# Performance work log

Measured on AMD Instinct MI355X. Metric: run time of the kernel, lower is better.

The kernel has to match this reference:

```python
import jax, jax.numpy as jnp
import numpy as np

B = 64
D_MODEL = 2048
D_SSM = 4096      # expand * d_model
HEADDIM = 64
NHEADS = 64       # D_SSM // HEADDIM
D_STATE = 128
D_IN_PROJ = 2 * D_SSM + 2 * D_STATE + NHEADS  # 8512, d_mlp == 0
ACT_LEVELS = 2 ** (8 - 1) - 1  # 127
W_LEVELS = 2 ** (8 - 1) - 1


def fake_quant(x, levels):
    # symmetric absmax fake-quant along last dim with straight-through estimator
    scale = jnp.max(jnp.abs(x), axis=-1, keepdims=True) / levels
    scale = jnp.where(scale == 0, 1.0, scale)
    q = jnp.round(x / scale) * scale
    return x + jax.lax.stop_gradient(q - x)


def quant_linear(x, W):
    # QuantLinear: fake-quant activations (per row) and weights (per output channel)
    xq = fake_quant(x, ACT_LEVELS)
    Wq = fake_quant(W, W_LEVELS)
    return xq @ Wq.T


def softplus_taylor3(x):
    return jnp.log(2.0) + 0.5 * x + x ** 2 / 8.0 + x ** 3 / 48.0


def exp_taylor5(x):
    return 1.0 + x + x ** 2 / 2.0 + x ** 3 / 6.0 + x ** 4 / 24.0 + x ** 5 / 120.0


def setup_inputs() -> dict:
    key = jax.random.key(0)
    k = jax.random.split(key, 7)
    hidden_states = jax.random.normal(k[0], (B, 1, D_MODEL), dtype=jnp.float32)
    ssm_state = jax.random.normal(k[1], (B, NHEADS, HEADDIM, D_STATE), dtype=jnp.float32) * 0.1
    W_in = jax.random.normal(k[2], (D_IN_PROJ, D_MODEL), dtype=jnp.float32) * (1.0 / np.sqrt(D_MODEL))
    # dt_bias = inverse-softplus of dt ~ LogUniform(1e-3, 1e-1)
    dt = jnp.exp(jax.random.uniform(k[3], (NHEADS,)) * (np.log(0.1) - np.log(0.001)) + np.log(0.001))
    dt_bias = dt + jnp.log(-jnp.expm1(-dt))
    A_log = jnp.log(jax.random.uniform(k[4], (NHEADS,), minval=1.0, maxval=16.0))
    Dp = jnp.ones((D_SSM,), dtype=jnp.float32)
    W_out = jax.random.normal(k[5], (D_MODEL, D_SSM), dtype=jnp.float32) * (1.0 / np.sqrt(D_SSM))
    return {"hidden_states": hidden_states, "ssm_state": ssm_state, "W_in": W_in,
            "dt_bias": dt_bias, "A_log": A_log, "D": Dp, "W_out": W_out}


def reference(hidden_states, ssm_state, W_in, dt_bias, A_log, D, W_out):
    dtype = hidden_states.dtype
    b = hidden_states.shape[0]
    zxbcdt = quant_linear(hidden_states[:, 0, :], W_in)  # [b, 8512]
    z = zxbcdt[:, :D_SSM]
    xBC = zxbcdt[:, D_SSM:2 * D_SSM + 2 * D_STATE]
    dt = zxbcdt[:, -NHEADS:]
    # activation fake-quant on xBC (STE)
    xBC = fake_quant(xBC, ACT_LEVELS)
    x = xBC[:, :D_SSM]                                   # [b, d_ssm]
    Bm = xBC[:, D_SSM:D_SSM + D_STATE]                   # [b, n]
    C = xBC[:, D_SSM + D_STATE:]                         # [b, n]
    A = -jnp.exp(A_log.astype(jnp.float32))              # [h]
    # no_sftplus: piecewise 3rd-order Taylor softplus
    dt = dt + dt_bias.astype(dt.dtype)
    dt = jnp.where(dt < -2.0, 0.0, jnp.where(dt > 2.0, dt, softplus_taylor3(dt)))
    # taylor_exp: clipped 5th-order Taylor exp of dt*A
    dA = jnp.maximum(dt * A, -10000.0)
    scale = jnp.clip(exp_taylor5(dA), 0.0, 1.0)          # [b, h]
    xh = x.reshape(b, NHEADS, HEADDIM)                   # [b, h, p]
    dBx = jnp.einsum('bh,bn,bhp->bhpn', dt, Bm, xh)
    ssm_state = ssm_state * scale[:, :, None, None] + dBx  # [b, h, p, n]
    y = jnp.einsum('bhpn,bn->bhp', ssm_state.astype(dtype), C).reshape(b, D_SSM)
    y = fake_quant(y, ACT_LEVELS)
    y = y + D.astype(dtype) * x                          # per-channel skip (D has d_ssm entries)
    y = y * jax.nn.relu(z)
    y = fake_quant(y, ACT_LEVELS)
    out = quant_linear(y, W_out)                         # [b, d_model]
    return out[:, None, :]
```

## Files before the change

### kernel.cpp

```cpp
#include <hip/hip_runtime.h>


#define B_       64
#define DMODEL   2048
#define DSSM     4096
#define NH       64
#define HD       64
#define DSTATE   128
#define DPROJ    8512
#define XBCLEN   4352

typedef __attribute__((ext_vector_type(8))) short short8;
typedef __attribute__((ext_vector_type(4))) float floatx4;

__device__ __forceinline__ float blockMax256(float v, float* sm) {
  #pragma unroll
  for (int off = 32; off > 0; off >>= 1)
    v = fmaxf(v, __shfl_xor(v, off, 64));
  __syncthreads();
  if ((threadIdx.x & 63) == 0) sm[threadIdx.x >> 6] = v;
  __syncthreads();
  return fmaxf(fmaxf(sm[0], sm[1]), fmaxf(sm[2], sm[3]));
}

__device__ __forceinline__ unsigned short bf16_of_int(float q) {
  return (unsigned short)(__float_as_uint(q) >> 16);
}

template<int COLS>
__global__ __launch_bounds__(256) void quant_rows(const float* __restrict__ in,
                                                  unsigned short* __restrict__ outq,
                                                  float* __restrict__ scales) {
  __shared__ float sm[4];
  constexpr int NV = COLS / 1024;
  int r = blockIdx.x;
  const float4* row = (const float4*)(in + (size_t)r * COLS);
  float4 v[NV];
  float m = 0.f;
  #pragma unroll
  for (int i = 0; i < NV; i++) {
    v[i] = row[threadIdx.x + i * 256];
    m = fmaxf(m, fmaxf(fmaxf(fabsf(v[i].x), fabsf(v[i].y)),
                       fmaxf(fabsf(v[i].z), fabsf(v[i].w))));
  }
  float s = blockMax256(m, sm) * (1.0f / 127.0f);
  if (s == 0.f) s = 1.f;
  if (threadIdx.x == 0) scales[r] = s;
  unsigned short* orow = outq + (size_t)r * COLS;
  #pragma unroll
  for (int i = 0; i < NV; i++) {
    int idx = (threadIdx.x + i * 256) * 4;
    ushort4 o;
    o.x = bf16_of_int(rintf(v[i].x / s));
    o.y = bf16_of_int(rintf(v[i].y / s));
    o.z = bf16_of_int(rintf(v[i].z / s));
    o.w = bf16_of_int(rintf(v[i].w / s));
    *(ushort4*)(orow + idx) = o;
  }
}

__global__ __launch_bounds__(256) void gemm_q(
    const unsigned short* __restrict__ A, int lda, const float* __restrict__ sA,
    const unsigned short* __restrict__ Bq, int ldb, const float* __restrict__ sB,
    float* __restrict__ Cout, int N, int kchunk) {
  int wave = threadIdx.x >> 6;
  int lane = threadIdx.x & 63;
  int l16 = lane & 15, quad = lane >> 4;
  int n0 = blockIdx.x * 64 + wave * 16;
  int k0 = blockIdx.y * kchunk;
  floatx4 zero = {0.f, 0.f, 0.f, 0.f};
  floatx4 acc[4] = {zero, zero, zero, zero};
  const unsigned short* brow = Bq + (size_t)(n0 + l16) * ldb;
  for (int k = k0; k < k0 + kchunk; k += 32) {
    int koff = k + quad * 8;
    short8 bfrag = *(const short8*)(brow + koff);
    #pragma unroll
    for (int mt = 0; mt < 4; mt++) {
      short8 afrag = *(const short8*)(A + (size_t)(mt * 16 + l16) * lda + koff);
      acc[mt] = __builtin_amdgcn_mfma_f32_16x16x32_bf16(afrag, bfrag, acc[mt], 0, 0, 0);
    }
  }
  int ncol = n0 + l16;
  float sb = sB[ncol];
  #pragma unroll
  for (int mt = 0; mt < 4; mt++) {
    #pragma unroll
    for (int r = 0; r < 4; r++) {
      int m = mt * 16 + quad * 4 + r;
      atomicAdd(&Cout[(size_t)m * N + ncol], acc[mt][r] * sA[m] * sb);
    }
  }
}

__global__ __launch_bounds__(256) void kxbc(const float* __restrict__ zxb,
                                            float* __restrict__ xbcq) {
  __shared__ float sm[4];
  int b = blockIdx.x;
  const float* row = zxb + (size_t)b * DPROJ + DSSM;
  float4 v[5];
  float m = 0.f;
  #pragma unroll
  for (int i = 0; i < 5; i++) {
    int idx = threadIdx.x * 4 + i * 1024;
    if (idx < XBCLEN) {
      v[i] = *(const float4*)(row + idx);
      m = fmaxf(m, fmaxf(fmaxf(fabsf(v[i].x), fabsf(v[i].y)),
                         fmaxf(fabsf(v[i].z), fabsf(v[i].w))));
    }
  }
  float s = blockMax256(m, sm) * (1.0f / 127.0f);
  if (s == 0.f) s = 1.f;
  float* orow = xbcq + (size_t)b * XBCLEN;
  #pragma unroll
  for (int i = 0; i < 5; i++) {
    int idx = threadIdx.x * 4 + i * 1024;
    if (idx < XBCLEN) {
      float4 q;
      q.x = rintf(v[i].x / s) * s;
      q.y = rintf(v[i].y / s) * s;
      q.z = rintf(v[i].z / s) * s;
      q.w = rintf(v[i].w / s) * s;
      *(float4*)(orow + idx) = q;
    }
  }
}

__global__ __launch_bounds__(256) void ky(const float* __restrict__ state,
                                          const float* __restrict__ zxb,
                                          const float* __restrict__ xbcq,
                                          const float* __restrict__ dt_bias,
                                          const float* __restrict__ A_log,
                                          float* __restrict__ yraw) {
  __shared__ float sh[3];
  int h = blockIdx.x, b = blockIdx.y;
  int t = threadIdx.x;
  const float* xrow = xbcq + (size_t)b * XBCLEN;
  const float* Bv = xrow + DSSM;
  const float* Cv = xrow + DSSM + DSTATE;
  int nb = (t * 4) & 127;
  float4 c4 = *(const float4*)(Cv + nb);
  if (t < 64) {
    float p = Bv[t] * Cv[t] + Bv[t + 64] * Cv[t + 64];
    #pragma unroll
    for (int off = 32; off > 0; off >>= 1) p += __shfl_xor(p, off, 64);
    if (t == 0) sh[0] = p;
  } else if (t == 64) {
    float dtv = zxb[(size_t)b * DPROJ + (DPROJ - NH) + h] + dt_bias[h];
    if (dtv < -2.f) dtv = 0.f;
    else if (dtv <= 2.f)
      dtv = 0.6931471805599453f + 0.5f * dtv + dtv * dtv * (1.f / 8.f)
            + dtv * dtv * dtv * (1.f / 48.f);
    float A = -expf(A_log[h]);
    float dA = fmaxf(dtv * A, -10000.f);
    float e = 1.f + dA + dA * dA * (1.f / 2.f) + dA * dA * dA * (1.f / 6.f)
              + dA * dA * dA * dA * (1.f / 24.f)
              + dA * dA * dA * dA * dA * (1.f / 120.f);
    e = fminf(fmaxf(e, 0.f), 1.f);
    sh[1] = dtv; sh[2] = e;
  }
  __syncthreads();
  float coef = sh[1] * sh[0];
  float sc = sh[2];
  const float4* st = (const float4*)(state + ((size_t)b * NH + h) * (HD * DSTATE));
  #pragma unroll
  for (int it = 0; it < 8; it++) {
    float4 s4 = st[t + it * 256];
    float acc = s4.x * c4.x + s4.y * c4.y + s4.z * c4.z + s4.w * c4.w;
    #pragma unroll
    for (int off = 1; off < 32; off <<= 1) acc += __shfl_xor(acc, off, 64);
    if ((t & 31) == 0) {
      int p = it * 8 + (t >> 5);
      int d = h * HD + p;
      yraw[(size_t)b * DSSM + d] = sc * acc + coef * xrow[d];
    }
  }
}

__global__ __launch_bounds__(256) void kepi(const float* __restrict__ yraw,
                                            const float* __restrict__ zxb,
                                            const float* __restrict__ xbcq,
                                            const float* __restrict__ Dv,
                                            unsigned short* __restrict__ q3,
                                            float* __restrict__ sy) {
  __shared__ float sm[4];
  int b = blockIdx.x, t = threadIdx.x;
  const float* yrow = yraw + (size_t)b * DSSM;
  float4 yv[4];
  float m = 0.f;
  #pragma unroll
  for (int i = 0; i < 4; i++) {
    yv[i] = *(const float4*)(yrow + t * 4 + i * 1024);
    m = fmaxf(m, fmaxf(fmaxf(fabsf(yv[i].x), fabsf(yv[i].y)),
                       fmaxf(fabsf(yv[i].z), fabsf(yv[i].w))));
  }
  float s1 = blockMax256(m, sm) * (1.0f / 127.0f);
  if (s1 == 0.f) s1 = 1.f;
  float4 y3[4];
  float m2 = 0.f;
  #pragma unroll
  for (int i = 0; i < 4; i++) {
    int idx = t * 4 + i * 1024;
    float4 x4 = *(const float4*)(xbcq + (size_t)b * XBCLEN + idx);
    float4 z4 = *(const float4*)(zxb + (size_t)b * DPROJ + idx);
    float4 d4 = *(const float4*)(Dv + idx);
    float4 r;
    r.x = (rintf(yv[i].x / s1) * s1 + d4.x * x4.x) * fmaxf(z4.x, 0.f);
    r.y = (rintf(yv[i].y / s1) * s1 + d4.y * x4.y) * fmaxf(z4.y, 0.f);
    r.z = (rintf(yv[i].z / s1) * s1 + d4.z * x4.z) * fmaxf(z4.z, 0.f);
    r.w = (rintf(yv[i].w / s1) * s1 + d4.w * x4.w) * fmaxf(z4.w, 0.f);
    y3[i] = r;
    m2 = fmaxf(m2, fmaxf(fmaxf(fabsf(r.x), fabsf(r.y)),
                         fmaxf(fabsf(r.z), fabsf(r.w))));
  }
  float s3 = blockMax256(m2, sm) * (1.0f / 127.0f);
  if (s3 == 0.f) s3 = 1.f;
  if (t == 0) sy[b] = s3;
  unsigned short* orow = q3 + (size_t)b * DSSM;
  #pragma unroll
  for (int i = 0; i < 4; i++) {
    int idx = t * 4 + i * 1024;
    ushort4 o;
    o.x = bf16_of_int(rintf(y3[i].x / s3));
    o.y = bf16_of_int(rintf(y3[i].y / s3));
    o.z = bf16_of_int(rintf(y3[i].z / s3));
    o.w = bf16_of_int(rintf(y3[i].w / s3));
    *(ushort4*)(orow + idx) = o;
  }
}

extern "C" void kernel_launch(void* const* d_in, const int* in_sizes, int n_in,
                              void* d_out, int out_size, void* d_ws, size_t ws_size,
                              hipStream_t stream) {
  const float* hidden  = (const float*)d_in[0];
  const float* ssm     = (const float*)d_in[1];
  const float* W_in    = (const float*)d_in[2];
  const float* dt_bias = (const float*)d_in[3];
  const float* A_log   = (const float*)d_in[4];
  const float* Dv      = (const float*)d_in[5];
  const float* W_out   = (const float*)d_in[6];
  float* out = (float*)d_out;

  char* p = (char*)d_ws;
  auto alloc = [&](size_t bytes) {
    char* r = p;
    p += (bytes + 255) & ~(size_t)255;
    return r;
  };
  unsigned short* xq   = (unsigned short*)alloc((size_t)B_ * DMODEL * 2);
  unsigned short* winq = (unsigned short*)alloc((size_t)DPROJ * DMODEL * 2);
  unsigned short* woq  = (unsigned short*)alloc((size_t)DMODEL * DSSM * 2);
  unsigned short* q3   = (unsigned short*)alloc((size_t)B_ * DSSM * 2);
  float* sx   = (float*)alloc(B_ * 4);
  float* swin = (float*)alloc(DPROJ * 4);
  float* swo  = (float*)alloc(DMODEL * 4);
  float* sy   = (float*)alloc(B_ * 4);
  float* zxb  = (float*)alloc((size_t)B_ * DPROJ * 4);
  float* xbcq = (float*)alloc((size_t)B_ * XBCLEN * 4);
  float* yraw = (float*)alloc((size_t)B_ * DSSM * 4);

  quant_rows<DMODEL><<<B_, 256, 0, stream>>>(hidden, xq, sx);
  quant_rows<DMODEL><<<DPROJ, 256, 0, stream>>>(W_in, winq, swin);
  quant_rows<DSSM><<<DMODEL, 256, 0, stream>>>(W_out, woq, swo);
  hipMemsetAsync(zxb, 0, (size_t)B_ * DPROJ * 4, stream);
  gemm_q<<<dim3(DPROJ / 64, 4), 256, 0, stream>>>(xq, DMODEL, sx,
                                                  winq, DMODEL, swin,
                                                  zxb, DPROJ, DMODEL / 4);
  kxbc<<<B_, 256, 0, stream>>>(zxb, xbcq);
  ky<<<dim3(NH, B_), 256, 0, stream>>>(ssm, zxb, xbcq, dt_bias, A_log, yraw);
  kepi<<<B_, 256, 0, stream>>>(yraw, zxb, xbcq, Dv, q3, sy);
  hipMemsetAsync(out, 0, (size_t)B_ * DMODEL * 4, stream);
  gemm_q<<<dim3(DMODEL / 64, 8), 256, 0, stream>>>(q3, DSSM, sy,
                                                   woq, DSSM, swo,
                                                   out, DMODEL, DSSM / 8);
}
```

Baseline: 339.5 us.

## Replace atomic split-K with partial buffers, fuse quant launches, restructure SSM stage

Merges the three weight and activation quantization launches into one grid. The GEMMs now write split-K partials to separate buffers instead of using atomics with memsets, and the split factors go up to 8 and 16. A new mid kernel reduces the partials, quantizes xBC, and computes the per-head dt, decay and B·C coefficients once per batch row. A final kernel reduces the output partials. The GEMM also gains register prefetch of the next fragments, the y kernel is reshaped to 16-lane reductions, and divisions become reciprocal multiplies, which can shift rounding at exact .5 ties.

```diff
diff --git a/kernel.cpp b/kernel.cpp
--- a/kernel.cpp
+++ b/kernel.cpp
@@ -9,6 +9,8 @@
 #define DSTATE   128
 #define DPROJ    8512
 #define XBCLEN   4352
+#define KS1      8
+#define KS2      16
 
 typedef __attribute__((ext_vector_type(8))) short short8;
 typedef __attribute__((ext_vector_type(4))) float floatx4;
@@ -23,27 +25,30 @@
   return fmaxf(fmaxf(sm[0], sm[1]), fmaxf(sm[2], sm[3]));
 }
 
+__device__ __forceinline__ float absmax4(float4 v) {
+  return fmaxf(fmaxf(fabsf(v.x), fabsf(v.y)), fmaxf(fabsf(v.z), fabsf(v.w)));
+}
+
 __device__ __forceinline__ unsigned short bf16_of_int(float q) {
   return (unsigned short)(__float_as_uint(q) >> 16);
 }
 
 template<int COLS>
-__global__ __launch_bounds__(256) void quant_rows(const float* __restrict__ in,
-                                                  unsigned short* __restrict__ outq,
-                                                  float* __restrict__ scales) {
-  __shared__ float sm[4];
+__device__ __forceinline__ void qrow(const float* __restrict__ in,
+                                     unsigned short* __restrict__ outq,
+                                     float* __restrict__ scales, int r, float* sm) {
   constexpr int NV = COLS / 1024;
-  int r = blockIdx.x;
   const float4* row = (const float4*)(in + (size_t)r * COLS);
   float4 v[NV];
   float m = 0.f;
   #pragma unroll
   for (int i = 0; i < NV; i++) {
     v[i] = row[threadIdx.x + i * 256];
-    m = fmaxf(m, fmaxf(fmaxf(fabsf(v[i].x), fabsf(v[i].y)),
-                       fmaxf(fabsf(v[i].z), fabsf(v[i].w))));
-  }
-  float s = blockMax256(m, sm) * (1.0f / 127.0f);
+    m = fmaxf(m, absmax4(v[i]));
+  }
+  float mx = blockMax256(m, sm);
+  float s = mx * (1.0f / 127.0f);
+  float rs = (s == 0.f) ? 0.f : 127.0f / mx;
   if (s == 0.f) s = 1.f;
   if (threadIdx.x == 0) scales[r] = s;
   unsigned short* orow = outq + (size_t)r * COLS;
@@ -51,18 +56,31 @@
   for (int i = 0; i < NV; i++) {
     int idx = (threadIdx.x + i * 256) * 4;
     ushort4 o;
-    o.x = bf16_of_int(rintf(v[i].x / s));
-    o.y = bf16_of_int(rintf(v[i].y / s));
-    o.z = bf16_of_int(rintf(v[i].z / s));
-    o.w = bf16_of_int(rintf(v[i].w / s));
+    o.x = bf16_of_int(rintf(v[i].x * rs));
+    o.y = bf16_of_int(rintf(v[i].y * rs));
+    o.z = bf16_of_int(rintf(v[i].z * rs));
+    o.w = bf16_of_int(rintf(v[i].w * rs));
     *(ushort4*)(orow + idx) = o;
   }
+}
+
+__global__ __launch_bounds__(256) void kquant_all(
+    const float* __restrict__ hidden, const float* __restrict__ W_in,
+    const float* __restrict__ W_out,
+    unsigned short* __restrict__ xq, unsigned short* __restrict__ winq,
+    unsigned short* __restrict__ woq,
+    float* __restrict__ sx, float* __restrict__ swin, float* __restrict__ swo) {
+  __shared__ float sm[4];
+  int bid = blockIdx.x;
+  if (bid < DPROJ)                 qrow<DMODEL>(W_in, winq, swin, bid, sm);
+  else if (bid < DPROJ + DMODEL)   qrow<DSSM>(W_out, woq, swo, bid - DPROJ, sm);
+  else                             qrow<DMODEL>(hidden, xq, sx, bid - DPROJ - DMODEL, sm);
 }
 
 __global__ __launch_bounds__(256) void gemm_q(
     const unsigned short* __restrict__ A, int lda, const float* __restrict__ sA,
     const unsigned short* __restrict__ Bq, int ldb, const float* __restrict__ sB,
-    float* __restrict__ Cout, int N, int kchunk) {
+    float* __restrict__ Pout, int N, int kchunk) {
   int wave = threadIdx.x >> 6;
   int lane = threadIdx.x & 63;
   int l16 = lane & 15, quad = lane >> 4;
@@ -70,114 +88,148 @@
   int k0 = blockIdx.y * kchunk;
   floatx4 zero = {0.f, 0.f, 0.f, 0.f};
   floatx4 acc[4] = {zero, zero, zero, zero};
-  const unsigned short* brow = Bq + (size_t)(n0 + l16) * ldb;
+  const unsigned short* brow = Bq + (size_t)(n0 + l16) * ldb + quad * 8;
+  const unsigned short* arow = A + (size_t)l16 * lda + quad * 8;
+  short8 bnext = *(const short8*)(brow + k0);
+  short8 anext[4];
+  #pragma unroll
+  for (int mt = 0; mt < 4; mt++)
+    anext[mt] = *(const short8*)(arow + (size_t)mt * 16 * lda + k0);
   for (int k = k0; k < k0 + kchunk; k += 32) {
-    int koff = k + quad * 8;
-    short8 bfrag = *(const short8*)(brow + koff);
+    short8 bcur = bnext;
+    short8 acur[4] = {anext[0], anext[1], anext[2], anext[3]};
+    if (k + 32 < k0 + kchunk) {
+      bnext = *(const short8*)(brow + k + 32);
+      #pragma unroll
+      for (int mt = 0; mt < 4; mt++)
+        anext[mt] = *(const short8*)(arow + (size_t)mt * 16 * lda + k + 32);
+    }
     #pragma unroll
-    for (int mt = 0; mt < 4; mt++) {
-      short8 afrag = *(const short8*)(A + (size_t)(mt * 16 + l16) * lda + koff);
-      acc[mt] = __builtin_amdgcn_mfma_f32_16x16x32_bf16(afrag, bfrag, acc[mt], 0, 0, 0);
-    }
+    for (int mt = 0; mt < 4; mt++)
+      acc[mt] = __builtin_amdgcn_mfma_f32_16x16x32_bf16(acur[mt], bcur, acc[mt], 0, 0, 0);
   }
   int ncol = n0 + l16;
   float sb = sB[ncol];
+  float* pbase = Pout + (size_t)blockIdx.y * 64 * N;
   #pragma unroll
   for (int mt = 0; mt < 4; mt++) {
     #pragma unroll
     for (int r = 0; r < 4; r++) {
       int m = mt * 16 + quad * 4 + r;
-      atomicAdd(&Cout[(size_t)m * N + ncol], acc[mt][r] * sA[m] * sb);
-    }
-  }
-}
-
-__global__ __launch_bounds__(256) void kxbc(const float* __restrict__ zxb,
-                                            float* __restrict__ xbcq) {
+      pbase[(size_t)m * N + ncol] = acc[mt][r] * sA[m] * sb;
+    }
+  }
+}
+
+__global__ __launch_bounds__(256) void kmid(
+    const float* __restrict__ P1, const float* __restrict__ dt_bias,
+    const float* __restrict__ A_log,
+    float* __restrict__ zbuf, float* __restrict__ xbcq, float* __restrict__ coefs) {
   __shared__ float sm[4];
-  int b = blockIdx.x;
-  const float* row = zxb + (size_t)b * DPROJ + DSSM;
-  float4 v[5];
+  __shared__ float dts[NH];
+  __shared__ float sbc;
+  int b = blockIdx.x, t = threadIdx.x;
+  float4 v[9];
   float m = 0.f;
   #pragma unroll
-  for (int i = 0; i < 5; i++) {
-    int idx = threadIdx.x * 4 + i * 1024;
-    if (idx < XBCLEN) {
-      v[i] = *(const float4*)(row + idx);
-      m = fmaxf(m, fmaxf(fmaxf(fabsf(v[i].x), fabsf(v[i].y)),
-                         fmaxf(fabsf(v[i].z), fabsf(v[i].w))));
-    }
-  }
-  float s = blockMax256(m, sm) * (1.0f / 127.0f);
+  for (int i = 0; i < 9; i++) {
+    int idx = t + i * 256;
+    if (idx < 2128) {
+      const float4* p0 = (const float4*)P1 + (size_t)b * 2128 + idx;
+      float4 a = p0[0];
+      #pragma unroll
+      for (int s = 1; s < KS1; s++) {
+        float4 q = p0[(size_t)s * 64 * 2128];
+        a.x += q.x; a.y += q.y; a.z += q.z; a.w += q.w;
+      }
+      v[i] = a;
+      if (idx >= 1024 && idx < 2112) m = fmaxf(m, absmax4(a));
+      if (idx >= 2112) {
+        dts[(t - 64) * 4 + 0] = a.x;
+        dts[(t - 64) * 4 + 1] = a.y;
+        dts[(t - 64) * 4 + 2] = a.z;
+        dts[(t - 64) * 4 + 3] = a.w;
+      }
+    }
+  }
+  float mx = blockMax256(m, sm);
+  float s = mx * (1.0f / 127.0f);
+  float rs = (s == 0.f) ? 0.f : 127.0f / mx;
   if (s == 0.f) s = 1.f;
-  float* orow = xbcq + (size_t)b * XBCLEN;
-  #pragma unroll
-  for (int i = 0; i < 5; i++) {
-    int idx = threadIdx.x * 4 + i * 1024;
-    if (idx < XBCLEN) {
+  float4 q8 = {0.f, 0.f, 0.f, 0.f};
+  #pragma unroll
+  for (int i = 0; i < 9; i++) {
+    int idx = t + i * 256;
+    if (idx < 1024) {
+      *((float4*)(zbuf + (size_t)b * DSSM) + idx) = v[i];
+    } else if (idx < 2112) {
       float4 q;
-      q.x = rintf(v[i].x / s) * s;
-      q.y = rintf(v[i].y / s) * s;
-      q.z = rintf(v[i].z / s) * s;
-      q.w = rintf(v[i].w / s) * s;
-      *(float4*)(orow + idx) = q;
-    }
-  }
-}
-
-__global__ __launch_bounds__(256) void ky(const float* __restrict__ state,
-                                          const float* __restrict__ zxb,
-                                          const float* __restrict__ xbcq,
-                                          const float* __restrict__ dt_bias,
-                                          const float* __restrict__ A_log,
-                                          float* __restrict__ yraw) {
-  __shared__ float sh[3];
-  int h = blockIdx.x, b = blockIdx.y;
-  int t = threadIdx.x;
-  const float* xrow = xbcq + (size_t)b * XBCLEN;
-  const float* Bv = xrow + DSSM;
-  const float* Cv = xrow + DSSM + DSTATE;
-  int nb = (t * 4) & 127;
-  float4 c4 = *(const float4*)(Cv + nb);
-  if (t < 64) {
-    float p = Bv[t] * Cv[t] + Bv[t + 64] * Cv[t + 64];
-    #pragma unroll
-    for (int off = 32; off > 0; off >>= 1) p += __shfl_xor(p, off, 64);
-    if (t == 0) sh[0] = p;
-  } else if (t == 64) {
-    float dtv = zxb[(size_t)b * DPROJ + (DPROJ - NH) + h] + dt_bias[h];
+      q.x = rintf(v[i].x * rs) * s;
+      q.y = rintf(v[i].y * rs) * s;
+      q.z = rintf(v[i].z * rs) * s;
+      q.w = rintf(v[i].w * rs) * s;
+      if (i == 8) q8 = q;
+      *((float4*)(xbcq + (size_t)b * XBCLEN) + (idx - 1024)) = q;
+    }
+  }
+  float4 oth;
+  oth.x = __shfl(q8.x, (t & 63) ^ 32, 64);
+  oth.y = __shfl(q8.y, (t & 63) ^ 32, 64);
+  oth.z = __shfl(q8.z, (t & 63) ^ 32, 64);
+  oth.w = __shfl(q8.w, (t & 63) ^ 32, 64);
+  float p = 0.f;
+  if (t < 32) p = q8.x * oth.x + q8.y * oth.y + q8.z * oth.z + q8.w * oth.w;
+  #pragma unroll
+  for (int off = 1; off < 32; off <<= 1) p += __shfl_xor(p, off, 64);
+  if (t == 0) sbc = p;
+  __syncthreads();
+  if (t < NH) {
+    float dtv = dts[t] + dt_bias[t];
     if (dtv < -2.f) dtv = 0.f;
     else if (dtv <= 2.f)
       dtv = 0.6931471805599453f + 0.5f * dtv + dtv * dtv * (1.f / 8.f)
             + dtv * dtv * dtv * (1.f / 48.f);
-    float A = -expf(A_log[h]);
+    float A = -expf(A_log[t]);
     float dA = fmaxf(dtv * A, -10000.f);
     float e = 1.f + dA + dA * dA * (1.f / 2.f) + dA * dA * dA * (1.f / 6.f)
               + dA * dA * dA * dA * (1.f / 24.f)
               + dA * dA * dA * dA * dA * (1.f / 120.f);
     e = fminf(fmaxf(e, 0.f), 1.f);
-    sh[1] = dtv; sh[2] = e;
-  }
-  __syncthreads();
-  float coef = sh[1] * sh[0];
-  float sc = sh[2];
+    coefs[((size_t)b * NH + t) * 2 + 0] = e;
+    coefs[((size_t)b * NH + t) * 2 + 1] = dtv * sbc;
+  }
+}
+
+__global__ __launch_bounds__(256) void ky(const float* __restrict__ state,
+                                          const float* __restrict__ xbcq,
+                                          const float* __restrict__ coefs,
+                                          float* __restrict__ yraw) {
+  int h = blockIdx.x, b = blockIdx.y, t = threadIdx.x;
+  const float* xrow = xbcq + (size_t)b * XBCLEN;
+  const float* Cv = xrow + DSSM + DSTATE;
+  int nc = (t & 15) * 8;
+  float4 c4a = *(const float4*)(Cv + nc);
+  float4 c4b = *(const float4*)(Cv + nc + 4);
+  float2 cf = *(const float2*)(coefs + ((size_t)b * NH + h) * 2);
   const float4* st = (const float4*)(state + ((size_t)b * NH + h) * (HD * DSTATE));
   #pragma unroll
-  for (int it = 0; it < 8; it++) {
-    float4 s4 = st[t + it * 256];
-    float acc = s4.x * c4.x + s4.y * c4.y + s4.z * c4.z + s4.w * c4.w;
+  for (int j = 0; j < 4; j++) {
+    int r = j * 16 + (t >> 4);
+    int base = r * 32 + (t & 15) * 2;
+    float4 s0 = st[base], s1 = st[base + 1];
+    float acc = s0.x * c4a.x + s0.y * c4a.y + s0.z * c4a.z + s0.w * c4a.w
+              + s1.x * c4b.x + s1.y * c4b.y + s1.z * c4b.z + s1.w * c4b.w;
     #pragma unroll
-    for (int off = 1; off < 32; off <<= 1) acc += __shfl_xor(acc, off, 64);
-    if ((t & 31) == 0) {
-      int p = it * 8 + (t >> 5);
-      int d = h * HD + p;
-      yraw[(size_t)b * DSSM + d] = sc * acc + coef * xrow[d];
+    for (int off = 1; off < 16; off <<= 1) acc += __shfl_xor(acc, off, 64);
+    if ((t & 15) == 0) {
+      int d = h * HD + r;
+      yraw[(size_t)b * DSSM + d] = cf.x * acc + cf.y * xrow[d];
     }
   }
 }
 
 __global__ __launch_bounds__(256) void kepi(const float* __restrict__ yraw,
-                                            const float* __restrict__ zxb,
+                                            const float* __restrict__ zbuf,
                                             const float* __restrict__ xbcq,
                                             const float* __restrict__ Dv,
                                             unsigned short* __restrict__ q3,
@@ -190,10 +242,11 @@
   #pragma unroll
   for (int i = 0; i < 4; i++) {
     yv[i] = *(const float4*)(yrow + t * 4 + i * 1024);
-    m = fmaxf(m, fmaxf(fmaxf(fabsf(yv[i].x), fabsf(yv[i].y)),
-                       fmaxf(fabsf(yv[i].z), fabsf(yv[i].w))));
-  }
-  float s1 = blockMax256(m, sm) * (1.0f / 127.0f);
+    m = fmaxf(m, absmax4(yv[i]));
+  }
+  float mx1 = blockMax256(m, sm);
+  float s1 = mx1 * (1.0f / 127.0f);
+  float rs1 = (s1 == 0.f) ? 0.f : 127.0f / mx1;
   if (s1 == 0.f) s1 = 1.f;
   float4 y3[4];
   float m2 = 0.f;
@@ -201,18 +254,19 @@
   for (int i = 0; i < 4; i++) {
     int idx = t * 4 + i * 1024;
     float4 x4 = *(const float4*)(xbcq + (size_t)b * XBCLEN + idx);
-    float4 z4 = *(const float4*)(zxb + (size_t)b * DPROJ + idx);
+    float4 z4 = *(const float4*)(zbuf + (size_t)b * DSSM + idx);
     float4 d4 = *(const float4*)(Dv + idx);
     float4 r;
-    r.x = (rintf(yv[i].x / s1) * s1 + d4.x * x4.x) * fmaxf(z4.x, 0.f);
-    r.y = (rintf(yv[i].y / s1) * s1 + d4.y * x4.y) * fmaxf(z4.y, 0.f);
-    r.z = (rintf(yv[i].z / s1) * s1 + d4.z * x4.z) * fmaxf(z4.z, 0.f);
-    r.w = (rintf(yv[i].w / s1) * s1 + d4.w * x4.w) * fmaxf(z4.w, 0.f);
+    r.x = (rintf(yv[i].x * rs1) * s1 + d4.x * x4.x) * fmaxf(z4.x, 0.f);
+    r.y = (rintf(yv[i].y * rs1) * s1 + d4.y * x4.y) * fmaxf(z4.y, 0.f);
+    r.z = (rintf(yv[i].z * rs1) * s1 + d4.z * x4.z) * fmaxf(z4.z, 0.f);
+    r.w = (rintf(yv[i].w * rs1) * s1 + d4.w * x4.w) * fmaxf(z4.w, 0.f);
     y3[i] = r;
-    m2 = fmaxf(m2, fmaxf(fmaxf(fabsf(r.x), fabsf(r.y)),
-                         fmaxf(fabsf(r.z), fabsf(r.w))));
-  }
-  float s3 = blockMax256(m2, sm) * (1.0f / 127.0f);
+    m2 = fmaxf(m2, absmax4(r));
+  }
+  float mx3 = blockMax256(m2, sm);
+  float s3 = mx3 * (1.0f / 127.0f);
+  float rs3 = (s3 == 0.f) ? 0.f : 127.0f / mx3;
   if (s3 == 0.f) s3 = 1.f;
   if (t == 0) sy[b] = s3;
   unsigned short* orow = q3 + (size_t)b * DSSM;
@@ -220,12 +274,25 @@
   for (int i = 0; i < 4; i++) {
     int idx = t * 4 + i * 1024;
     ushort4 o;
-    o.x = bf16_of_int(rintf(y3[i].x / s3));
-    o.y = bf16_of_int(rintf(y3[i].y / s3));
-    o.z = bf16_of_int(rintf(y3[i].z / s3));
-    o.w = bf16_of_int(rintf(y3[i].w / s3));
+    o.x = bf16_of_int(rintf(y3[i].x * rs3));
+    o.y = bf16_of_int(rintf(y3[i].y * rs3));
+    o.z = bf16_of_int(rintf(y3[i].z * rs3));
+    o.w = bf16_of_int(rintf(y3[i].w * rs3));
     *(ushort4*)(orow + idx) = o;
   }
+}
+
+__global__ __launch_bounds__(256) void kout(const float* __restrict__ P2,
+                                            float* __restrict__ out) {
+  int idx = blockIdx.x * 256 + threadIdx.x;
+  const float4* p = (const float4*)P2;
+  float4 s = p[idx];
+  #pragma unroll
+  for (int i = 1; i < KS2; i++) {
+    float4 a = p[(size_t)i * 32768 + idx];
+    s.x += a.x; s.y += a.y; s.z += a.z; s.w += a.w;
+  }
+  ((float4*)out)[idx] = s;
 }
 
 extern "C" void kernel_launch(void* const* d_in, const int* in_sizes, int n_in,
@@ -250,26 +317,27 @@
   unsigned short* winq = (unsigned short*)alloc((size_t)DPROJ * DMODEL * 2);
   unsigned short* woq  = (unsigned short*)alloc((size_t)DMODEL * DSSM * 2);
   unsigned short* q3   = (unsigned short*)alloc((size_t)B_ * DSSM * 2);
-  float* sx   = (float*)alloc(B_ * 4);
-  float* swin = (float*)alloc(DPROJ * 4);
-  float* swo  = (float*)alloc(DMODEL * 4);
-  float* sy   = (float*)alloc(B_ * 4);
-  float* zxb  = (float*)alloc((size_t)B_ * DPROJ * 4);
-  float* xbcq = (float*)alloc((size_t)B_ * XBCLEN * 4);
-  float* yraw = (float*)alloc((size_t)B_ * DSSM * 4);
-
-  quant_rows<DMODEL><<<B_, 256, 0, stream>>>(hidden, xq, sx);
-  quant_rows<DMODEL><<<DPROJ, 256, 0, stream>>>(W_in, winq, swin);
-  quant_rows<DSSM><<<DMODEL, 256, 0, stream>>>(W_out, woq, swo);
-  hipMemsetAsync(zxb, 0, (size_t)B_ * DPROJ * 4, stream);
-  gemm_q<<<dim3(DPROJ / 64, 4), 256, 0, stream>>>(xq, DMODEL, sx,
-                                                  winq, DMODEL, swin,
-                                                  zxb, DPROJ, DMODEL / 4);
-  kxbc<<<B_, 256, 0, stream>>>(zxb, xbcq);
-  ky<<<dim3(NH, B_), 256, 0, stream>>>(ssm, zxb, xbcq, dt_bias, A_log, yraw);
-  kepi<<<B_, 256, 0, stream>>>(yraw, zxb, xbcq, Dv, q3, sy);
-  hipMemsetAsync(out, 0, (size_t)B_ * DMODEL * 4, stream);
-  gemm_q<<<dim3(DMODEL / 64, 8), 256, 0, stream>>>(q3, DSSM, sy,
-                                                   woq, DSSM, swo,
-                                                   out, DMODEL, DSSM / 8);
-}
+  float* sx    = (float*)alloc(B_ * 4);
+  float* swin  = (float*)alloc(DPROJ * 4);
+  float* swo   = (float*)alloc(DMODEL * 4);
+  float* sy    = (float*)alloc(B_ * 4);
+  float* P1    = (float*)alloc((size_t)KS1 * B_ * DPROJ * 4);
+  float* P2    = (float*)alloc((size_t)KS2 * B_ * DMODEL * 4);
+  float* zbuf  = (float*)alloc((size_t)B_ * DSSM * 4);
+  float* xbcq  = (float*)alloc((size_t)B_ * XBCLEN * 4);
+  float* coefs = (float*)alloc((size_t)B_ * NH * 2 * 4);
+  float* yraw  = (float*)alloc((size_t)B_ * DSSM * 4);
+
+  kquant_all<<<DPROJ + DMODEL + B_, 256, 0, stream>>>(hidden, W_in, W_out,
+                                                      xq, winq, woq, sx, swin, swo);
+  gemm_q<<<dim3(DPROJ / 64, KS1), 256, 0, stream>>>(xq, DMODEL, sx,
+                                                    winq, DMODEL, swin,
+                                                    P1, DPROJ, DMODEL / KS1);
+  kmid<<<B_, 256, 0, stream>>>(P1, dt_bias, A_log, zbuf, xbcq, coefs);
+  ky<<<dim3(NH, B_), 256, 0, stream>>>(ssm, xbcq, coefs, yraw);
+  kepi<<<B_, 256, 0, stream>>>(yraw, zbuf, xbcq, Dv, q3, sy);
+  gemm_q<<<dim3(DMODEL / 64, KS2), 256, 0, stream>>>(q3, DSSM, sy,
+                                                     woq, DSSM, swo,
+                                                     P2, DMODEL, DSSM / KS2);
+  kout<<<DMODEL / 16, 256, 0, stream>>>(P2, out);
+}
```

Measured after the change: 324.3 us. 4.5% less time.
